# Kernel tuning notes

Hardware: AMD Instinct MI355X
Metric: run time of the kernel (lower is better)

The kernel has to match this reference:

```python
import jax, jax.numpy as jnp
import numpy as np

N = 8192
IN_F = 300
OUT_F = 300
ALPHA = 0.3  # leaky relu slope
NEG_INF = -1e12


def setup_inputs() -> dict:
    key = jax.random.key(0)
    k1, k2, k3, k4, k5 = jax.random.split(key, 5)
    inp = jax.random.normal(k1, (N, IN_F), dtype=jnp.float32)
    adj = jax.random.randint(k2, (N, N), 0, 2, dtype=jnp.int32)
    # xavier-uniform-like init for params
    def xavier(k, shape):
        fan_in, fan_out = shape[0], shape[1]
        limit = 1.414 * (6.0 / (fan_in + fan_out)) ** 0.5
        return jax.random.uniform(k, shape, jnp.float32, -limit, limit)
    W = xavier(k3, (IN_F, OUT_F))
    a = xavier(k4, (2 * OUT_F, 1))
    wtrans = xavier(k5, (2 * IN_F, OUT_F))
    return {"inp": inp, "adj": adj, "W": W, "a": a, "wtrans": wtrans}


def reference(inp, adj, W, a, wtrans):
    # h: [N, OUT_F]
    h = inp @ W
    Wh1 = h @ a[:OUT_F, :]          # [N, 1]
    Wh2 = h @ a[OUT_F:, :]          # [N, 1]
    e = jax.nn.leaky_relu(Wh1 + Wh2.T, negative_slope=ALPHA)  # [N, N]
    mask = adj > 0
    attention = jax.nn.softmax(jnp.where(mask, e, NEG_INF), axis=1)
    negative_attention = -jax.nn.softmax(jnp.where(mask, -e, NEG_INF), axis=1)
    # dropout p=0.0 / eval mode -> identity
    h_prime = attention @ inp                 # [N, IN_F]
    h_prime_negative = negative_attention @ inp
    h_prime_double = jnp.concatenate([h_prime, h_prime_negative], axis=1)  # [N, 2*IN_F]
    new_h_prime = h_prime_double @ wtrans     # [N, OUT_F]
    return jax.nn.elu(new_h_prime)  # concat=True
```

## Files before the change

kernel.cpp:

```cpp
#include <hip/hip_runtime.h>
#include <stdint.h>

#define NROW 8192
#define LOG2E 1.4426950408889634f
#define ALPHA 0.3f

#define WA1_OFF 0
#define WA2_OFF 512
#define S1_OFF 1024
#define S2_OFF (1024 + 8192)
#define SCAL_OFF (S2_OFF + 8192)
#define PQB_OFF 70656
#define PQB_BYTES (256 * 40960)
#define AMSK_OFF (PQB_OFF + PQB_BYTES)
#define AMSK_BYTES (NROW * 256 * 4)
#define WTF_OFF (AMSK_OFF + AMSK_BYTES)
#define WTF_BYTES (10 * 40960)
#define PART_OFF (WTF_OFF + WTF_BYTES)

typedef _Float16 f16x8 __attribute__((ext_vector_type(8)));
typedef __fp16 fp16x2 __attribute__((ext_vector_type(2)));
typedef float f32x4 __attribute__((ext_vector_type(4)));

union HPack { fp16x2 h2[4]; f16x8 v; uint32_t u[4]; };
union PkU { fp16x2 p; uint32_t u; };

__device__ __forceinline__ int swz(int col, int g) { return (g + (col >> 1)) & 3; }

__global__ void k_wa(const float* __restrict__ Wm, const float* __restrict__ a,
                     float* __restrict__ wsf) {
  int r = blockIdx.x * 4 + (threadIdx.x >> 6);
  int ln = threadIdx.x & 63;
  if (r >= 300) return;
  float a1 = 0.f, a2 = 0.f;
  for (int c = ln; c < 300; c += 64) {
    float w = Wm[r * 300 + c];
    a1 += w * a[c];
    a2 += w * a[300 + c];
  }
  for (int o = 32; o; o >>= 1) { a1 += __shfl_down(a1, o); a2 += __shfl_down(a2, o); }
  if (!ln) { wsf[WA1_OFF + r] = a1; wsf[WA2_OFF + r] = a2; }
}

__global__ void k_s12(const float* __restrict__ inp, float* __restrict__ wsf) {
  int row = blockIdx.x * 4 + (threadIdx.x >> 6);
  int ln = threadIdx.x & 63;
  const float* ip = inp + (size_t)row * 300;
  float a1 = 0.f, a2 = 0.f;
  for (int c = ln; c < 300; c += 64) {
    float v = ip[c];
    a1 += v * wsf[WA1_OFF + c];
    a2 += v * wsf[WA2_OFF + c];
  }
  for (int o = 32; o; o >>= 1) { a1 += __shfl_down(a1, o); a2 += __shfl_down(a2, o); }
  if (!ln) { wsf[S1_OFF + row] = a1 * LOG2E; wsf[S2_OFF + row] = a2 * LOG2E; }
}

__global__ void k_minmax(float* __restrict__ wsf) {
  int t = threadIdx.x;
  float mx = -3e38f, mn = 3e38f;
  for (int i = t; i < NROW; i += 1024) {
    float v = wsf[S2_OFF + i];
    mx = fmaxf(mx, v); mn = fminf(mn, v);
  }
  for (int o = 32; o; o >>= 1) {
    mx = fmaxf(mx, __shfl_down(mx, o));
    mn = fminf(mn, __shfl_down(mn, o));
  }
  __shared__ float sm[32];
  int wv = t >> 6, ln = t & 63;
  if (!ln) { sm[wv] = mx; sm[16 + wv] = mn; }
  __syncthreads();
  if (!t) {
    float M = sm[0], m = sm[16];
    for (int q = 1; q < 16; q++) { M = fmaxf(M, sm[q]); m = fminf(m, sm[16 + q]); }
    wsf[SCAL_OFF] = M; wsf[SCAL_OFF + 1] = m;
  }
}

__global__ __launch_bounds__(320) void k_wprep(const float* __restrict__ wt,
                                               uint16_t* __restrict__ wtf) {
  const int t = blockIdx.x >> 1;
  const int pq = blockIdx.x & 1;
  const int col = threadIdx.x;
  uint16_t* dst = wtf + (size_t)t * 20480 + pq * 10240 + col * 32;
  #pragma unroll
  for (int g = 0; g < 4; g++) {
    const int gs = swz(col, g);
    uint32_t* d32 = (uint32_t*)(dst + gs * 8);
    #pragma unroll
    for (int jj = 0; jj < 4; jj++) {
      const int c0 = t * 32 + g * 8 + 2 * jj;
      float v0 = (col < 300 && c0 < 300) ? wt[(size_t)(pq * 300 + c0) * 300 + col] : 0.f;
      float v1 = (col < 300 && c0 + 1 < 300) ? wt[(size_t)(pq * 300 + c0 + 1) * 300 + col] : 0.f;
      PkU pk; pk.p = __builtin_amdgcn_cvt_pkrtz(v0, v1);
      d32[jj] = pk.u;
    }
  }
}

#define WT_BLOCKS 256
__global__ __launch_bounds__(640) void k_packwt(const int* __restrict__ adj,
                                                uint32_t* __restrict__ amask,
                                                const float* __restrict__ inp,
                                                const uint16_t* __restrict__ wtf,
                                                uint16_t* __restrict__ pqb) {
  __shared__ __align__(16) uint16_t W2[2][20480];
  const int bid = blockIdx.x;
  const int tid = threadIdx.x;
  if (bid >= WT_BLOCKS) {
    const size_t wd = (size_t)(bid - WT_BLOCKS) * 640 + tid;
    if (wd < (size_t)NROW * 256) {
      const int4* src = (const int4*)(adj + wd * 32);
      uint32_t m = 0;
      #pragma unroll
      for (int j = 0; j < 8; j++) {
        int4 v = src[j];
        m |= (v.x ? 1u : 0u) << (4 * j);
        m |= (v.y ? 1u : 0u) << (4 * j + 1);
        m |= (v.z ? 1u : 0u) << (4 * j + 2);
        m |= (v.w ? 1u : 0u) << (4 * j + 3);
      }
      amask[wd] = m;
    }
    return;
  }
  const int kb = bid;
  const int w = tid >> 6, lane = tid & 63;
  const int lr = lane & 15, lg = lane >> 4;
  const int side = (w >= 5) ? 1 : 0;
  const int w5 = w - side * 5;
  f32x4 acc[2][4];
  const f32x4 zero = {0.f, 0.f, 0.f, 0.f};
  #pragma unroll
  for (int fr = 0; fr < 2; fr++)
    #pragma unroll
    for (int i = 0; i < 4; i++) acc[fr][i] = zero;

  auto STAGE = [&](int b, int t) {
    const char* tile = (const char*)wtf + (size_t)t * 40960;
    char* dst = (char*)W2[b];
    #pragma unroll
    for (int it = 0; it < 4; it++) {
      const int off = (w * 4 + it) * 1024;
      __builtin_amdgcn_global_load_lds(
          (const __attribute__((address_space(1))) void*)(tile + off + lane * 16),
          (__attribute__((address_space(3))) void*)(dst + off),
          16, 0, 0);
    }
  };

  const float* arow0 = inp + (size_t)(kb * 32 + lr) * 300;
  const float* arow1 = inp + (size_t)(kb * 32 + 16 + lr) * 300;

  STAGE(0, 0);
  __syncthreads();
  for (int t = 0; t < 10; t++) {
    if (t < 9) STAGE((t + 1) & 1, t + 1);
    const int c = t * 32 + lg * 8;
    float4 z4 = {0.f, 0.f, 0.f, 0.f};
    float4 a0l = z4, a0h = z4, a1l = z4, a1h = z4;
    if (c <= 296) { a0l = *(const float4*)(arow0 + c); a1l = *(const float4*)(arow1 + c); }
    if (c <= 292) { a0h = *(const float4*)(arow0 + c + 4); a1h = *(const float4*)(arow1 + c + 4); }
    HPack A0, A1;
    A0.h2[0] = __builtin_amdgcn_cvt_pkrtz(a0l.x, a0l.y);
    A0.h2[1] = __builtin_amdgcn_cvt_pkrtz(a0l.z, a0l.w);
    A0.h2[2] = __builtin_amdgcn_cvt_pkrtz(a0h.x, a0h.y);
    A0.h2[3] = __builtin_amdgcn_cvt_pkrtz(a0h.z, a0h.w);
    A1.h2[0] = __builtin_amdgcn_cvt_pkrtz(a1l.x, a1l.y);
    A1.h2[1] = __builtin_amdgcn_cvt_pkrtz(a1l.z, a1l.w);
    A1.h2[2] = __builtin_amdgcn_cvt_pkrtz(a1h.x, a1h.y);
    A1.h2[3] = __builtin_amdgcn_cvt_pkrtz(a1h.z, a1h.w);
    const char* half = (const char*)W2[t & 1] + side * 20480;
    #pragma unroll
    for (int i = 0; i < 4; i++) {
      const int f = w5 * 4 + i;
      if (f < 19) {
        const int col = f * 16 + lr;
        f16x8 b = *(const f16x8*)(half + col * 64 + swz(col, lg) * 16);
        acc[0][i] = __builtin_amdgcn_mfma_f32_16x16x32_f16(A0.v, b, acc[0][i], 0, 0, 0);
        acc[1][i] = __builtin_amdgcn_mfma_f32_16x16x32_f16(A1.v, b, acc[1][i], 0, 0, 0);
      }
    }
    __syncthreads();
  }
  uint16_t* outb = pqb + (size_t)kb * 20480 + side * 10240;
  #pragma unroll
  for (int i = 0; i < 4; i++) {
    const int f = w5 * 4 + i;
    if (f >= 19) continue;
    const int col = f * 16 + lr;
    #pragma unroll
    for (int fr = 0; fr < 2; fr++) {
      float v0 = acc[fr][i][0], v1 = acc[fr][i][1], v2 = acc[fr][i][2], v3 = acc[fr][i][3];
      if (col == 300) { v0 = v1 = v2 = v3 = 1.0f; }
      else if (col > 300) { v0 = v1 = v2 = v3 = 0.0f; }
      const int g = fr * 2 + (lg >> 1);
      uint32_t* dst = (uint32_t*)(outb + col * 32 + swz(col, g) * 8 + (lg & 1) * 4);
      PkU p0; p0.p = __builtin_amdgcn_cvt_pkrtz(v0, v1);
      PkU p1; p1.p = __builtin_amdgcn_cvt_pkrtz(v2, v3);
      dst[0] = p0.u;
      dst[1] = p1.u;
    }
  }
}

__global__ __launch_bounds__(256, 2) void k_main(const uint32_t* __restrict__ amask,
                                                 const float* __restrict__ wsf,
                                                 const uint16_t* __restrict__ pqb,
                                                 float* __restrict__ part, int nsplit) {
  __shared__ __align__(16) uint16_t Bsm[2][20480];
  const int bid = blockIdx.x;
  const int mblk = bid / nsplit;
  const int ks = bid - mblk * nsplit;
  const int tid = threadIdx.x;
  const int w = tid >> 6, lane = tid & 63;
  const int lr = lane & 15, lg = lane >> 4;
  const int side = w & 1;
  const int rg = w >> 1;
  const int rbase = mblk * 64 + rg * 32;
  const int row0 = rbase + lr;
  const int row1 = rbase + 16 + lr;
  const float c1_0 = wsf[S1_OFF + row0];
  const float c1_1 = wsf[S1_OFF + row1];
  const float s2ref = side ? wsf[SCAL_OFF + 1] : wsf[SCAL_OFF];
  const float sgn = side ? -1.0f : 1.0f;
  float tt0 = c1_0 + s2ref; const float so0 = sgn * fmaxf(tt0, ALPHA * tt0);
  float tt1 = c1_1 + s2ref; const float so1 = sgn * fmaxf(tt1, ALPHA * tt1);
  const int kcnt = NROW / nsplit;
  const int k0 = ks * kcnt;
  const int ksteps = kcnt >> 5;
  const int tb0 = k0 >> 5;
  const uint32_t* mr0 = amask + (size_t)row0 * 256;
  const uint32_t* mr1 = amask + (size_t)row1 * 256;
  f32x4 acc0[19], acc1[19];
  const f32x4 zero = {0.f, 0.f, 0.f, 0.f};
  #pragma unroll
  for (int ct = 0; ct < 19; ct++) { acc0[ct] = zero; acc1[ct] = zero; }

  auto STAGE = [&](int b, int tb) {
    const char* tile = (const char*)(pqb + (size_t)tb * 20480);
    char* dst = (char*)Bsm[b];
    #pragma unroll
    for (int it = 0; it < 10; it++) {
      const int off = (w * 10 + it) * 1024;
      __builtin_amdgcn_global_load_lds(
          (const __attribute__((address_space(1))) void*)(tile + off + lane * 16),
          (__attribute__((address_space(3))) void*)(dst + off),
          16, 0, 0);
    }
  };

  STAGE(0, tb0);
  uint32_t cM0 = mr0[tb0];
  uint32_t cM1 = mr1[tb0];
  const int kw0 = k0 + lg * 8;
  float4 cS0 = *(const float4*)(wsf + S2_OFF + kw0);
  float4 cS1 = *(const float4*)(wsf + S2_OFF + kw0 + 4);

  for (int s = 0; s < ksteps; s++) {
    const int sp = (s + 1 < ksteps) ? s + 1 : s;
    const uint32_t nM0 = mr0[tb0 + sp];
    const uint32_t nM1 = mr1[tb0 + sp];
    const int kwn = k0 + sp * 32 + lg * 8;
    const float4 nS0 = *(const float4*)(wsf + S2_OFF + kwn);
    const float4 nS1 = *(const float4*)(wsf + S2_OFF + kwn + 4);

    asm volatile("s_waitcnt vmcnt(4)" ::: "memory");
    __builtin_amdgcn_sched_barrier(0);
    __builtin_amdgcn_s_barrier();

    STAGE((s + 1) & 1, tb0 + sp);

    float se[8] = {cS0.x, cS0.y, cS0.z, cS0.w, cS1.x, cS1.y, cS1.z, cS1.w};
    const uint32_t b0 = (cM0 >> (lg * 8)) & 0xffu;
    const uint32_t b1 = (cM1 >> (lg * 8)) & 0xffu;
    HPack up0, up1;
    #pragma unroll
    for (int e = 0; e < 8; e += 2) {
      float e0a = c1_0 + se[e];     e0a = fmaxf(e0a, ALPHA * e0a);
      float e0b = c1_0 + se[e + 1]; e0b = fmaxf(e0b, ALPHA * e0b);
      float e1a = c1_1 + se[e];     e1a = fmaxf(e1a, ALPHA * e1a);
      float e1b = c1_1 + se[e + 1]; e1b = fmaxf(e1b, ALPHA * e1b);
      float p0a = exp2f(__builtin_fmaf(sgn, e0a, -so0)); p0a = (b0 & (1u << e)) ? p0a : 0.0f;
      float p0b = exp2f(__builtin_fmaf(sgn, e0b, -so0)); p0b = (b0 & (2u << e)) ? p0b : 0.0f;
      float p1a = exp2f(__builtin_fmaf(sgn, e1a, -so1)); p1a = (b1 & (1u << e)) ? p1a : 0.0f;
      float p1b = exp2f(__builtin_fmaf(sgn, e1b, -so1)); p1b = (b1 & (2u << e)) ? p1b : 0.0f;
      up0.h2[e >> 1] = __builtin_amdgcn_cvt_pkrtz(p0a, p0b);
      up1.h2[e >> 1] = __builtin_amdgcn_cvt_pkrtz(p1a, p1b);
    }

    const char* half = (const char*)Bsm[s & 1] + side * 20480;
    __builtin_amdgcn_s_setprio(1);
    #pragma unroll
    for (int ct = 0; ct < 19; ct++) {
      const int col = ct * 16 + lr;
      const int gp = swz(col, lg);
      f16x8 b = *(const f16x8*)(half + col * 64 + gp * 16);
      acc0[ct] = __builtin_amdgcn_mfma_f32_16x16x32_f16(up0.v, b, acc0[ct], 0, 0, 0);
      acc1[ct] = __builtin_amdgcn_mfma_f32_16x16x32_f16(up1.v, b, acc1[ct], 0, 0, 0);
    }
    __builtin_amdgcn_s_setprio(0);

    cM0 = nM0; cM1 = nM1; cS0 = nS0; cS1 = nS1;
  }

  float* pb = part + ((size_t)ks * NROW + rbase) * 608 + (size_t)side * 304;
  #pragma unroll
  for (int ct = 0; ct < 19; ct++) {
    const int col = ct * 16 + lr;
    #pragma unroll
    for (int r = 0; r < 4; r++) {
      pb[(size_t)(lg * 4 + r) * 608 + col] = acc0[ct][r];
      pb[(size_t)(16 + lg * 4 + r) * 608 + col] = acc1[ct][r];
    }
  }
}

__global__ void k_final(const float* __restrict__ part, float* __restrict__ out, int nsplit) {
  const int i = blockIdx.x;
  const int t = threadIdx.x;
  if (t >= 300) return;
  float sp = 0.f, sn = 0.f, zp = 0.f, zn = 0.f;
  for (int s = 0; s < nsplit; s++) {
    const float* p = part + ((size_t)s * NROW + i) * 608;
    sp += p[t];
    sn += p[304 + t];
    zp += p[300];
    zn += p[604];
  }
  float x = sp / zp - sn / zn;
  out[(size_t)i * 300 + t] = (x > 0.f) ? x : (exp2f(x * LOG2E) - 1.0f);
}

extern "C" void kernel_launch(void* const* d_in, const int* in_sizes, int n_in,
                              void* d_out, int out_size, void* d_ws, size_t ws_size,
                              hipStream_t stream) {
  const float* inp = (const float*)d_in[0];
  const int* adj = (const int*)d_in[1];
  const float* Wm = (const float*)d_in[2];
  const float* a = (const float*)d_in[3];
  const float* wt = (const float*)d_in[4];
  float* out = (float*)d_out;
  float* wsf = (float*)d_ws;
  uint16_t* pqb = (uint16_t*)((char*)d_ws + PQB_OFF);
  uint32_t* amask = (uint32_t*)((char*)d_ws + AMSK_OFF);
  uint16_t* wtf = (uint16_t*)((char*)d_ws + WTF_OFF);
  float* part = (float*)((char*)d_ws + PART_OFF);

  int nsplit = 4;
  while (nsplit > 1 &&
         (size_t)PART_OFF + (size_t)nsplit * NROW * 608 * 4 > ws_size)
    nsplit >>= 1;

  const int pack_blocks = (NROW * 256 + 639) / 640;
  k_wa<<<75, 256, 0, stream>>>(Wm, a, wsf);
  k_wprep<<<20, 320, 0, stream>>>(wt, wtf);
  k_s12<<<NROW / 4, 256, 0, stream>>>(inp, wsf);
  k_minmax<<<1, 1024, 0, stream>>>(wsf);
  k_packwt<<<WT_BLOCKS + pack_blocks, 640, 0, stream>>>(adj, amask, inp, wtf, pqb);
  k_main<<<128 * nsplit, 256, 0, stream>>>(amask, wsf, pqb, part, nsplit);
  k_final<<<NROW, 320, 0, stream>>>(part, out, nsplit);
}
```

Baseline: 231.6 us.

## Load B fragments directly from global into registers, split sides across blocks

The main kernel stops staging the packed feature tile into LDS through global_load_lds with double buffering and barriers. Each lane now loads its B fragments straight from global memory into registers, prefetching the next k-step while the MFMAs for the current step run. The positive and negative attention sides move from separate waves to separate blocks, so each block has four row groups of 32 rows for one side. This drops the LDS traffic and the block barriers, but every wave now fetches its own B tile, which raises global/L2 traffic. It also adds 19 more vector registers per lane, and launch_bounds no longer requests two blocks per CU.

```diff
diff --git a/kernel.cpp b/kernel.cpp
--- a/kernel.cpp
+++ b/kernel.cpp
@@ -205,20 +205,20 @@
   }
 }
 
-__global__ __launch_bounds__(256, 2) void k_main(const uint32_t* __restrict__ amask,
-                                                 const float* __restrict__ wsf,
-                                                 const uint16_t* __restrict__ pqb,
-                                                 float* __restrict__ part, int nsplit) {
-  __shared__ __align__(16) uint16_t Bsm[2][20480];
+__global__ __launch_bounds__(256) void k_main(const uint32_t* __restrict__ amask,
+                                              const float* __restrict__ wsf,
+                                              const uint16_t* __restrict__ pqb,
+                                              float* __restrict__ part, int nsplit) {
   const int bid = blockIdx.x;
-  const int mblk = bid / nsplit;
-  const int ks = bid - mblk * nsplit;
+  const int nsg = 2 * nsplit;
+  const int sub = bid % nsg;
+  const int side = sub & 1;
+  const int ks = sub >> 1;
+  const int mgrp = bid / nsg;
   const int tid = threadIdx.x;
   const int w = tid >> 6, lane = tid & 63;
   const int lr = lane & 15, lg = lane >> 4;
-  const int side = w & 1;
-  const int rg = w >> 1;
-  const int rbase = mblk * 64 + rg * 32;
+  const int rbase = mgrp * 128 + w * 32;
   const int row0 = rbase + lr;
   const int row1 = rbase + 16 + lr;
   const float c1_0 = wsf[S1_OFF + row0];
@@ -228,53 +228,38 @@
   float tt0 = c1_0 + s2ref; const float so0 = sgn * fmaxf(tt0, ALPHA * tt0);
   float tt1 = c1_1 + s2ref; const float so1 = sgn * fmaxf(tt1, ALPHA * tt1);
   const int kcnt = NROW / nsplit;
+  const int ksteps = kcnt >> 5;
   const int k0 = ks * kcnt;
-  const int ksteps = kcnt >> 5;
   const int tb0 = k0 >> 5;
   const uint32_t* mr0 = amask + (size_t)row0 * 256;
   const uint32_t* mr1 = amask + (size_t)row1 * 256;
+  const int gs = (lg + (lr >> 1)) & 3;
+  const int laneoff = lr * 64 + gs * 16;
+  const char* pqbase = (const char*)pqb + (size_t)side * 20480 + laneoff;
+
   f32x4 acc0[19], acc1[19];
   const f32x4 zero = {0.f, 0.f, 0.f, 0.f};
   #pragma unroll
   for (int ct = 0; ct < 19; ct++) { acc0[ct] = zero; acc1[ct] = zero; }
 
-  auto STAGE = [&](int b, int tb) {
-    const char* tile = (const char*)(pqb + (size_t)tb * 20480);
-    char* dst = (char*)Bsm[b];
-    #pragma unroll
-    for (int it = 0; it < 10; it++) {
-      const int off = (w * 10 + it) * 1024;
-      __builtin_amdgcn_global_load_lds(
-          (const __attribute__((address_space(1))) void*)(tile + off + lane * 16),
-          (__attribute__((address_space(3))) void*)(dst + off),
-          16, 0, 0);
-    }
-  };
-
-  STAGE(0, tb0);
-  uint32_t cM0 = mr0[tb0];
-  uint32_t cM1 = mr1[tb0];
-  const int kw0 = k0 + lg * 8;
-  float4 cS0 = *(const float4*)(wsf + S2_OFF + kw0);
-  float4 cS1 = *(const float4*)(wsf + S2_OFF + kw0 + 4);
+  f16x8 bv[19];
+  {
+    const char* b0 = pqbase + (size_t)tb0 * 40960;
+    #pragma unroll
+    for (int ct = 0; ct < 19; ct++) bv[ct] = *(const f16x8*)(b0 + ct * 1024);
+  }
 
   for (int s = 0; s < ksteps; s++) {
-    const int sp = (s + 1 < ksteps) ? s + 1 : s;
-    const uint32_t nM0 = mr0[tb0 + sp];
-    const uint32_t nM1 = mr1[tb0 + sp];
-    const int kwn = k0 + sp * 32 + lg * 8;
-    const float4 nS0 = *(const float4*)(wsf + S2_OFF + kwn);
-    const float4 nS1 = *(const float4*)(wsf + S2_OFF + kwn + 4);
-
-    asm volatile("s_waitcnt vmcnt(4)" ::: "memory");
-    __builtin_amdgcn_sched_barrier(0);
-    __builtin_amdgcn_s_barrier();
-
-    STAGE((s + 1) & 1, tb0 + sp);
-
-    float se[8] = {cS0.x, cS0.y, cS0.z, cS0.w, cS1.x, cS1.y, cS1.z, cS1.w};
-    const uint32_t b0 = (cM0 >> (lg * 8)) & 0xffu;
-    const uint32_t b1 = (cM1 >> (lg * 8)) & 0xffu;
+    const int tb = tb0 + s;
+    const uint32_t m0 = mr0[tb];
+    const uint32_t m1 = mr1[tb];
+    const int kw = (tb << 5) + lg * 8;
+    const float4 s0 = *(const float4*)(wsf + S2_OFF + kw);
+    const float4 s1v = *(const float4*)(wsf + S2_OFF + kw + 4);
+
+    float se[8] = {s0.x, s0.y, s0.z, s0.w, s1v.x, s1v.y, s1v.z, s1v.w};
+    const uint32_t b0m = (m0 >> (lg * 8)) & 0xffu;
+    const uint32_t b1m = (m1 >> (lg * 8)) & 0xffu;
     HPack up0, up1;
     #pragma unroll
     for (int e = 0; e < 8; e += 2) {
@@ -282,27 +267,23 @@
       float e0b = c1_0 + se[e + 1]; e0b = fmaxf(e0b, ALPHA * e0b);
       float e1a = c1_1 + se[e];     e1a = fmaxf(e1a, ALPHA * e1a);
       float e1b = c1_1 + se[e + 1]; e1b = fmaxf(e1b, ALPHA * e1b);
-      float p0a = exp2f(__builtin_fmaf(sgn, e0a, -so0)); p0a = (b0 & (1u << e)) ? p0a : 0.0f;
-      float p0b = exp2f(__builtin_fmaf(sgn, e0b, -so0)); p0b = (b0 & (2u << e)) ? p0b : 0.0f;
-      float p1a = exp2f(__builtin_fmaf(sgn, e1a, -so1)); p1a = (b1 & (1u << e)) ? p1a : 0.0f;
-      float p1b = exp2f(__builtin_fmaf(sgn, e1b, -so1)); p1b = (b1 & (2u << e)) ? p1b : 0.0f;
+      float p0a = exp2f(__builtin_fmaf(sgn, e0a, -so0)); p0a = (b0m & (1u << e)) ? p0a : 0.0f;
+      float p0b = exp2f(__builtin_fmaf(sgn, e0b, -so0)); p0b = (b0m & (2u << e)) ? p0b : 0.0f;
+      float p1a = exp2f(__builtin_fmaf(sgn, e1a, -so1)); p1a = (b1m & (1u << e)) ? p1a : 0.0f;
+      float p1b = exp2f(__builtin_fmaf(sgn, e1b, -so1)); p1b = (b1m & (2u << e)) ? p1b : 0.0f;
       up0.h2[e >> 1] = __builtin_amdgcn_cvt_pkrtz(p0a, p0b);
       up1.h2[e >> 1] = __builtin_amdgcn_cvt_pkrtz(p1a, p1b);
     }
 
-    const char* half = (const char*)Bsm[s & 1] + side * 20480;
-    __builtin_amdgcn_s_setprio(1);
+    const int tn = (s + 1 < ksteps) ? tb + 1 : tb;
+    const char* nb = pqbase + (size_t)tn * 40960;
     #pragma unroll
     for (int ct = 0; ct < 19; ct++) {
-      const int col = ct * 16 + lr;
-      const int gp = swz(col, lg);
-      f16x8 b = *(const f16x8*)(half + col * 64 + gp * 16);
+      f16x8 b = bv[ct];
       acc0[ct] = __builtin_amdgcn_mfma_f32_16x16x32_f16(up0.v, b, acc0[ct], 0, 0, 0);
       acc1[ct] = __builtin_amdgcn_mfma_f32_16x16x32_f16(up1.v, b, acc1[ct], 0, 0, 0);
-    }
-    __builtin_amdgcn_s_setprio(0);
-
-    cM0 = nM0; cM1 = nM1; cS0 = nS0; cS1 = nS1;
+      bv[ct] = *(const f16x8*)(nb + ct * 1024);
+    }
   }
 
   float* pb = part + ((size_t)ks * NROW + rbase) * 608 + (size_t)side * 304;
@@ -359,6 +340,6 @@
   k_s12<<<NROW / 4, 256, 0, stream>>>(inp, wsf);
   k_minmax<<<1, 1024, 0, stream>>>(wsf);
   k_packwt<<<WT_BLOCKS + pack_blocks, 640, 0, stream>>>(adj, amask, inp, wtf, pqb);
-  k_main<<<128 * nsplit, 256, 0, stream>>>(amask, wsf, pqb, part, nsplit);
+  k_main<<<(NROW / 128) * 2 * nsplit, 256, 0, stream>>>(amask, wsf, pqb, part, nsplit);
   k_final<<<NROW, 320, 0, stream>>>(part, out, nsplit);
 }
```

New measurement: 247.3 us. 1.07x slower.
